# Performance work log

Hardware: AMD Instinct MI355X
Metric: run time of the kernel (lower is better)

The kernel has to match this reference:

```python
import jax, jax.numpy as jnp
import numpy as np

B, L, D, V, O = 512, 256, 256, 100000, 1000  # L must equal D (see MaxPool1d(kernel_size=D) + squeeze)


def setup_inputs() -> dict:
    key = jax.random.key(0)
    k1, k2, k3, k4, k5 = jax.random.split(key, 5)
    input_sentence = jax.random.randint(k1, (B, L), 0, V)
    emb_weight = jax.random.normal(k2, (V, D), dtype=jnp.float32) * 0.02
    # xavier_uniform for W_b: bound = sqrt(6/(D+D))
    bound = float(np.sqrt(6.0 / (D + D)))
    W_b = jax.random.uniform(k3, (D, D), dtype=jnp.float32, minval=-bound, maxval=bound)
    lw = float(np.sqrt(1.0 / D))
    lin_w = jax.random.uniform(k4, (O, D), dtype=jnp.float32, minval=-lw, maxval=lw)
    lin_b = jax.random.uniform(k5, (O,), dtype=jnp.float32, minval=-lw, maxval=lw)
    return {"input_sentence": input_sentence, "emb_weight": emb_weight,
            "W_b": W_b, "lin_w": lin_w, "lin_b": lin_b}


def reference(input_sentence, emb_weight, W_b, lin_w, lin_b):
    # Embedding lookup: [B, L, D]
    we = emb_weight[input_sentence]
    # torch stores embeddings as [B, D, L] then re-transposes inside the co-attention;
    # net effect: C = tanh(E W_b E^T) with E = [B, L, D]  ->  C: [B, L, L]
    C = jnp.tanh(jnp.einsum('bld,de,bme->blm', we, W_b, we))
    # Dropout(p=0.5) is identity in eval mode.
    # MaxPool1d(kernel_size=D) over last axis with L == D -> max over last dim, keepdims
    max_cow = jnp.max(C, axis=-1, keepdims=True)          # [B, L, 1]
    a_q = jax.nn.softmax(max_cow, axis=1)                  # softmax over L
    # bmm(a_q^T [B,1,L], E [B,L,D]) -> [B,1,D], then squeeze dim 1
    f_w = jnp.einsum('blo,bld->bod', a_q, we)[:, 0, :]     # [B, D]
    return f_w @ lin_w.T + lin_b                           # [B, O]
```

## Files before the change

### kernel.cpp

```cpp
#include <hip/hip_runtime.h>
#include <hip/hip_bf16.h>
#include <math.h>

#define B_ 512
#define L_ 256
#define D_ 256
#define V_ 100000
#define O_ 1000

typedef __attribute__((ext_vector_type(8))) short short8;
typedef __attribute__((ext_vector_type(4))) float f32x4;

static __device__ __forceinline__ unsigned short f2bf(float f) {
    union { float f; unsigned u; } v; v.f = f;
    unsigned r = v.u + 0x7FFFu + ((v.u >> 16) & 1u);
    return (unsigned short)(r >> 16);
}
static __device__ __forceinline__ float bf2f(unsigned short u) {
    union { unsigned u; float f; } v; v.u = ((unsigned)u) << 16;
    return v.f;
}

__global__ __launch_bounds__(256) void k_wt(const float* __restrict__ Wb,
                                            unsigned short* __restrict__ Wbf) {
    int i = blockIdx.x * 256 + threadIdx.x;
    Wbf[i] = f2bf(Wb[i]);
}

__global__ __launch_bounds__(512, 2) void k_attn(const int* __restrict__ tok,
                                                 const float* __restrict__ emb,
                                                 const unsigned short* __restrict__ Wbf,
                                                 float* __restrict__ fw) {
    __shared__ char lds[163840];
    char* EsC = lds;
    char* HtC = lds + 131072;
    float* red2    = (float*)(lds + 131072);
    float* scratch = (float*)(lds + 131072 + 1024);
    float* fred    = (float*)(lds + 131072 + 1152);

    int b = blockIdx.x;
    int tid = threadIdx.x;
    int wid = tid >> 6, ln = tid & 63;
    int l16 = ln & 15, gp = ln >> 4;

    {
        const int* tb = tok + (b << 8);
#pragma unroll
        for (int it = 0; it < 32; it++) {
            int row = it * 8 + wid;
            int t = tb[row];
            float4 v = *(const float4*)(emb + ((size_t)t << 8) + (ln << 2));
            unsigned long long pk;
            unsigned short* p = (unsigned short*)&pk;
            p[0] = f2bf(v.x); p[1] = f2bf(v.y); p[2] = f2bf(v.z); p[3] = f2bf(v.w);
            int byt = (row << 9) | ((ln << 3) ^ ((row & 7) << 4));
            *(unsigned long long*)(EsC + byt) = pk;
        }
    }

    int i0 = wid * 32;
    short8 wfr[8][2];
#pragma unroll
    for (int k = 0; k < 8; k++)
#pragma unroll
        for (int rf = 0; rf < 2; rf++)
            wfr[k][rf] = *(const short8*)(Wbf + ((i0 + rf * 16 + l16) << 8) + k * 32 + gp * 8);
    __syncthreads();

    int l0 = i0;
    short8 efr[8][2];
#pragma unroll
    for (int k = 0; k < 8; k++)
#pragma unroll
        for (int rf = 0; rf < 2; rf++) {
            int l = l0 + rf * 16 + l16;
            int byt = (l << 9) | ((k * 64 + gp * 16) ^ ((l & 7) << 4));
            efr[k][rf] = *(const short8*)(EsC + byt);
        }

    float rmax[8];
#pragma unroll
    for (int i = 0; i < 8; i++) rmax[i] = -1e30f;

    for (int mt = 0; mt < 4; mt++) {
        int m0 = mt * 64;
        {
            f32x4 acc[2][4] = {};
#pragma unroll
            for (int k0 = 0; k0 < 256; k0 += 32) {
                int kk2 = (k0 + gp * 8) * 2;
                short8 bfr[4];
#pragma unroll
                for (int cf = 0; cf < 4; cf++) {
                    int jg = m0 + cf * 16 + l16;
                    int byt = (jg << 9) | (kk2 ^ ((jg & 7) << 4));
                    bfr[cf] = *(const short8*)(EsC + byt);
                }
                int ks = k0 >> 5;
#pragma unroll
                for (int rf = 0; rf < 2; rf++)
#pragma unroll
                    for (int cf = 0; cf < 4; cf++)
                        acc[rf][cf] = __builtin_amdgcn_mfma_f32_16x16x32_bf16(
                            wfr[ks][rf], bfr[cf], acc[rf][cf], 0, 0, 0);
            }
#pragma unroll
            for (int rf = 0; rf < 2; rf++)
#pragma unroll
                for (int cf = 0; cf < 4; cf++) {
                    int i = i0 + rf * 16 + gp * 4;
                    int jl = cf * 16 + l16;
                    unsigned long long pk;
                    unsigned short* p = (unsigned short*)&pk;
                    p[0] = f2bf(acc[rf][cf][0]);
                    p[1] = f2bf(acc[rf][cf][1]);
                    p[2] = f2bf(acc[rf][cf][2]);
                    p[3] = f2bf(acc[rf][cf][3]);
                    int byt = (jl << 9) | ((i * 2) ^ ((jl & 7) << 4));
                    *(unsigned long long*)(HtC + byt) = pk;
                }
        }
        __syncthreads();
        {
            f32x4 acc[2][4] = {};
#pragma unroll
            for (int k0 = 0; k0 < 256; k0 += 32) {
                int kk2 = (k0 + gp * 8) * 2;
                short8 bb[4];
#pragma unroll
                for (int cf = 0; cf < 4; cf++) {
                    int m = cf * 16 + l16;
                    int byt = (m << 9) | (kk2 ^ ((m & 7) << 4));
                    bb[cf] = *(const short8*)(HtC + byt);
                }
                int ks = k0 >> 5;
#pragma unroll
                for (int rf = 0; rf < 2; rf++)
#pragma unroll
                    for (int cf = 0; cf < 4; cf++)
                        acc[rf][cf] = __builtin_amdgcn_mfma_f32_16x16x32_bf16(
                            efr[ks][rf], bb[cf], acc[rf][cf], 0, 0, 0);
            }
#pragma unroll
            for (int rf = 0; rf < 2; rf++)
#pragma unroll
                for (int r = 0; r < 4; r++) {
                    float mx = fmaxf(fmaxf(acc[rf][0][r], acc[rf][1][r]),
                                     fmaxf(acc[rf][2][r], acc[rf][3][r]));
                    rmax[rf * 4 + r] = fmaxf(rmax[rf * 4 + r], mx);
                }
        }
        __syncthreads();
    }

#pragma unroll
    for (int i = 0; i < 8; i++) {
        float v = rmax[i];
        v = fmaxf(v, __shfl_xor(v, 1));
        v = fmaxf(v, __shfl_xor(v, 2));
        v = fmaxf(v, __shfl_xor(v, 4));
        v = fmaxf(v, __shfl_xor(v, 8));
        rmax[i] = v;
    }
    if (l16 == 0) {
#pragma unroll
        for (int rf = 0; rf < 2; rf++)
#pragma unroll
            for (int r = 0; r < 4; r++)
                red2[l0 + rf * 16 + gp * 4 + r] = rmax[rf * 4 + r];
    }
    __syncthreads();

    float x = -1e30f;
    if (tid < 256) x = tanhf(red2[tid]);
    float mx = x;
#pragma unroll
    for (int s = 1; s < 64; s <<= 1) mx = fmaxf(mx, __shfl_xor(mx, s));
    if (ln == 0) scratch[wid] = mx;
    __syncthreads();
    float bm = scratch[0];
#pragma unroll
    for (int i = 1; i < 8; i++) bm = fmaxf(bm, scratch[i]);
    float e = (tid < 256) ? expf(x - bm) : 0.f;
    float sm = e;
#pragma unroll
    for (int s = 1; s < 64; s <<= 1) sm += __shfl_xor(sm, s);
    if (ln == 0) scratch[8 + wid] = sm;
    __syncthreads();
    float tot = 0.f;
#pragma unroll
    for (int i = 0; i < 8; i++) tot += scratch[8 + i];
    if (tid < 256) red2[tid] = e / tot;
    __syncthreads();

    {
        int g = tid >> 5;
        int d0 = (tid & 31) << 3;
        float s0[8] = {0.f, 0.f, 0.f, 0.f, 0.f, 0.f, 0.f, 0.f};
        int lbase = g << 4;
#pragma unroll
        for (int li = 0; li < 16; li++) {
            int l = lbase + li;
            float aql = red2[l];
            int byt = (l << 9) | ((d0 * 2) ^ ((l & 7) << 4));
            short8 v = *(const short8*)(EsC + byt);
#pragma unroll
            for (int jj = 0; jj < 8; jj++)
                s0[jj] += aql * bf2f((unsigned short)v[jj]);
        }
        f32x4 w0, w1;
        w0[0] = s0[0]; w0[1] = s0[1]; w0[2] = s0[2]; w0[3] = s0[3];
        w1[0] = s0[4]; w1[1] = s0[5]; w1[2] = s0[6]; w1[3] = s0[7];
        *(f32x4*)(fred + g * 256 + d0) = w0;
        *(f32x4*)(fred + g * 256 + d0 + 4) = w1;
    }
    __syncthreads();
    if (tid < 256) {
        float f = 0.f;
#pragma unroll
        for (int g2 = 0; g2 < 16; g2++) f += fred[g2 * 256 + tid];
        fw[(b << 8) + tid] = f;
    }
}

__global__ __launch_bounds__(256) void k_out(const float* __restrict__ fw,
                                             const float* __restrict__ lw,
                                             const float* __restrict__ lb,
                                             float* __restrict__ out) {
    __shared__ float As[32][68];
    __shared__ float Bs[64][65];
    int tid = threadIdx.x;
    int tx = tid & 15, ty = tid >> 4;
    int r0 = blockIdx.y * 32, n0 = blockIdx.x * 64;
    float acc[2][4] = {};
    for (int k0 = 0; k0 < 256; k0 += 64) {
        __syncthreads();
#pragma unroll
        for (int it = 0; it < 2; it++) {
            int idx = it * 256 + tid;
            int i = idx >> 4, k4 = (idx & 15) << 2;
            *(float4*)&As[i][k4] = *(const float4*)&fw[(r0 + i) * 256 + k0 + k4];
        }
#pragma unroll
        for (int it = 0; it < 4; it++) {
            int idx = it * 256 + tid;
            int n = idx >> 4, k4 = (idx & 15) << 2;
            int nn = n0 + n;
            float4 v = {0.f, 0.f, 0.f, 0.f};
            if (nn < O_) v = *(const float4*)&lw[(size_t)nn * 256 + k0 + k4];
            Bs[k4][n] = v.x; Bs[k4 + 1][n] = v.y; Bs[k4 + 2][n] = v.z; Bs[k4 + 3][n] = v.w;
        }
        __syncthreads();
#pragma unroll
        for (int k = 0; k < 64; k++) {
            float a0 = As[ty * 2][k], a1 = As[ty * 2 + 1][k];
            float b0 = Bs[k][tx * 4], b1 = Bs[k][tx * 4 + 1];
            float b2 = Bs[k][tx * 4 + 2], b3 = Bs[k][tx * 4 + 3];
            acc[0][0] += a0 * b0; acc[0][1] += a0 * b1; acc[0][2] += a0 * b2; acc[0][3] += a0 * b3;
            acc[1][0] += a1 * b0; acc[1][1] += a1 * b1; acc[1][2] += a1 * b2; acc[1][3] += a1 * b3;
        }
    }
#pragma unroll
    for (int i = 0; i < 2; i++)
#pragma unroll
        for (int j = 0; j < 4; j++) {
            int n = n0 + tx * 4 + j;
            if (n < O_) out[(size_t)(r0 + ty * 2 + i) * O_ + n] = acc[i][j] + lb[n];
        }
}

extern "C" void kernel_launch(void* const* d_in, const int* in_sizes, int n_in,
                              void* d_out, int out_size, void* d_ws, size_t ws_size,
                              hipStream_t stream) {
    const int* tok = (const int*)d_in[0];
    const float* emb = (const float*)d_in[1];
    const float* Wb = (const float*)d_in[2];
    const float* lw = (const float*)d_in[3];
    const float* lb = (const float*)d_in[4];
    float* out = (float*)d_out;

    char* ws = (char*)d_ws;
    unsigned short* Wbf = (unsigned short*)(ws);
    float*          fwp = (float*)(ws + 131072);

    hipLaunchKernelGGL(k_wt,   dim3(256),    dim3(256), 0, stream, Wb, Wbf);
    hipLaunchKernelGGL(k_attn, dim3(512),    dim3(512), 0, stream, tok, emb, Wbf, fwp);
    hipLaunchKernelGGL(k_out,  dim3(16, 16), dim3(256), 0, stream, fwp, lw, lb, out);
}
```

Measured before the change: 79.87 us.

## Stream embedding tiles through double-buffered LDS and prefetch next tile during compute

Instead of staging all 256 embedding rows in LDS up front, the kernel loads 64-row tiles into a double buffer, prefetching the next tile's gather into registers while the current tile's MFMAs run. One barrier per tile is removed. The A-operand fragments now come straight from global memory with bf16 conversion, and the final weighted sum re-reads fp32 embeddings from global. This cuts LDS use, from 160KB to about 145KB, and hides gather latency. In exchange it adds global re-reads and register pressure, and the final pooling now uses fp32 rather than bf16 values.

```diff
diff --git a/kernel.cpp b/kernel.cpp
--- a/kernel.cpp
+++ b/kernel.cpp
@@ -31,59 +31,76 @@
                                                  const float* __restrict__ emb,
                                                  const unsigned short* __restrict__ Wbf,
                                                  float* __restrict__ fw) {
-    __shared__ char lds[163840];
-    char* EsC = lds;
-    char* HtC = lds + 131072;
+    __shared__ __align__(16) char lds[148544];
     float* red2    = (float*)(lds + 131072);
-    float* scratch = (float*)(lds + 131072 + 1024);
-    float* fred    = (float*)(lds + 131072 + 1152);
+    float* scratch = (float*)(lds + 132096);
+    float* fred    = (float*)(lds + 132160);
 
     int b = blockIdx.x;
     int tid = threadIdx.x;
     int wid = tid >> 6, ln = tid & 63;
     int l16 = ln & 15, gp = ln >> 4;
-
-    {
-        const int* tb = tok + (b << 8);
-#pragma unroll
-        for (int it = 0; it < 32; it++) {
-            int row = it * 8 + wid;
-            int t = tb[row];
-            float4 v = *(const float4*)(emb + ((size_t)t << 8) + (ln << 2));
-            unsigned long long pk;
-            unsigned short* p = (unsigned short*)&pk;
-            p[0] = f2bf(v.x); p[1] = f2bf(v.y); p[2] = f2bf(v.z); p[3] = f2bf(v.w);
-            int byt = (row << 9) | ((ln << 3) ^ ((row & 7) << 4));
-            *(unsigned long long*)(EsC + byt) = pk;
-        }
-    }
-
     int i0 = wid * 32;
+    const int* tb = tok + (b << 8);
+
+    float4 g4[8];
+#pragma unroll
+    for (int it = 0; it < 8; it++) {
+        int r = it * 8 + wid;
+        g4[it] = *(const float4*)(emb + ((size_t)tb[r] << 8) + (ln << 2));
+    }
     short8 wfr[8][2];
 #pragma unroll
     for (int k = 0; k < 8; k++)
 #pragma unroll
         for (int rf = 0; rf < 2; rf++)
             wfr[k][rf] = *(const short8*)(Wbf + ((i0 + rf * 16 + l16) << 8) + k * 32 + gp * 8);
-    __syncthreads();
-
-    int l0 = i0;
+    int trow0 = tb[i0 + l16];
+    int trow1 = tb[i0 + 16 + l16];
     short8 efr[8][2];
 #pragma unroll
     for (int k = 0; k < 8; k++)
 #pragma unroll
         for (int rf = 0; rf < 2; rf++) {
-            int l = l0 + rf * 16 + l16;
-            int byt = (l << 9) | ((k * 64 + gp * 16) ^ ((l & 7) << 4));
-            efr[k][rf] = *(const short8*)(EsC + byt);
-        }
+            const float4* sp = (const float4*)(emb + ((size_t)(rf ? trow1 : trow0) << 8) + k * 32 + gp * 8);
+            float4 a = sp[0], c = sp[1];
+            short8 o;
+            o[0] = (short)f2bf(a.x); o[1] = (short)f2bf(a.y);
+            o[2] = (short)f2bf(a.z); o[3] = (short)f2bf(a.w);
+            o[4] = (short)f2bf(c.x); o[5] = (short)f2bf(c.y);
+            o[6] = (short)f2bf(c.z); o[7] = (short)f2bf(c.w);
+            efr[k][rf] = o;
+        }
+#pragma unroll
+    for (int it = 0; it < 8; it++) {
+        int r = it * 8 + wid;
+        unsigned long long pk;
+        unsigned short* p = (unsigned short*)&pk;
+        p[0] = f2bf(g4[it].x); p[1] = f2bf(g4[it].y);
+        p[2] = f2bf(g4[it].z); p[3] = f2bf(g4[it].w);
+        *(unsigned long long*)(lds + ((r << 9) | ((ln << 3) ^ ((r & 7) << 4)))) = pk;
+    }
+    __syncthreads();
 
     float rmax[8];
 #pragma unroll
     for (int i = 0; i < 8; i++) rmax[i] = -1e30f;
 
+#pragma unroll
     for (int mt = 0; mt < 4; mt++) {
-        int m0 = mt * 64;
+        char* EtCur = lds + (mt & 1) * 32768;
+        char* EtNxt = lds + ((mt + 1) & 1) * 32768;
+        char* HtCur = lds + 65536 + (mt & 1) * 32768;
+
+        float4 ng[8];
+        if (mt < 3) {
+            int m0n = (mt + 1) * 64;
+#pragma unroll
+            for (int it = 0; it < 8; it++) {
+                int r = it * 8 + wid;
+                ng[it] = *(const float4*)(emb + ((size_t)tb[m0n + r] << 8) + (ln << 2));
+            }
+        }
         {
             f32x4 acc[2][4] = {};
 #pragma unroll
@@ -92,9 +109,8 @@
                 short8 bfr[4];
 #pragma unroll
                 for (int cf = 0; cf < 4; cf++) {
-                    int jg = m0 + cf * 16 + l16;
-                    int byt = (jg << 9) | (kk2 ^ ((jg & 7) << 4));
-                    bfr[cf] = *(const short8*)(EsC + byt);
+                    int jl = cf * 16 + l16;
+                    bfr[cf] = *(const short8*)(EtCur + ((jl << 9) | (kk2 ^ ((jl & 7) << 4))));
                 }
                 int ks = k0 >> 5;
 #pragma unroll
@@ -116,9 +132,19 @@
                     p[1] = f2bf(acc[rf][cf][1]);
                     p[2] = f2bf(acc[rf][cf][2]);
                     p[3] = f2bf(acc[rf][cf][3]);
-                    int byt = (jl << 9) | ((i * 2) ^ ((jl & 7) << 4));
-                    *(unsigned long long*)(HtC + byt) = pk;
+                    *(unsigned long long*)(HtCur + ((jl << 9) | ((i * 2) ^ ((jl & 7) << 4)))) = pk;
                 }
+        }
+        if (mt < 3) {
+#pragma unroll
+            for (int it = 0; it < 8; it++) {
+                int r = it * 8 + wid;
+                unsigned long long pk;
+                unsigned short* p = (unsigned short*)&pk;
+                p[0] = f2bf(ng[it].x); p[1] = f2bf(ng[it].y);
+                p[2] = f2bf(ng[it].z); p[3] = f2bf(ng[it].w);
+                *(unsigned long long*)(EtNxt + ((r << 9) | ((ln << 3) ^ ((r & 7) << 4)))) = pk;
+            }
         }
         __syncthreads();
         {
@@ -130,8 +156,7 @@
 #pragma unroll
                 for (int cf = 0; cf < 4; cf++) {
                     int m = cf * 16 + l16;
-                    int byt = (m << 9) | (kk2 ^ ((m & 7) << 4));
-                    bb[cf] = *(const short8*)(HtC + byt);
+                    bb[cf] = *(const short8*)(HtCur + ((m << 9) | (kk2 ^ ((m & 7) << 4))));
                 }
                 int ks = k0 >> 5;
 #pragma unroll
@@ -150,7 +175,6 @@
                     rmax[rf * 4 + r] = fmaxf(rmax[rf * 4 + r], mx);
                 }
         }
-        __syncthreads();
     }
 
 #pragma unroll
@@ -167,7 +191,7 @@
         for (int rf = 0; rf < 2; rf++)
 #pragma unroll
             for (int r = 0; r < 4; r++)
-                red2[l0 + rf * 16 + gp * 4 + r] = rmax[rf * 4 + r];
+                red2[i0 + rf * 16 + gp * 4 + r] = rmax[rf * 4 + r];
     }
     __syncthreads();
 
@@ -202,11 +226,10 @@
         for (int li = 0; li < 16; li++) {
             int l = lbase + li;
             float aql = red2[l];
-            int byt = (l << 9) | ((d0 * 2) ^ ((l & 7) << 4));
-            short8 v = *(const short8*)(EsC + byt);
-#pragma unroll
-            for (int jj = 0; jj < 8; jj++)
-                s0[jj] += aql * bf2f((unsigned short)v[jj]);
+            const float4* sp = (const float4*)(emb + ((size_t)tb[l] << 8) + d0);
+            float4 a = sp[0], c = sp[1];
+            s0[0] += aql * a.x; s0[1] += aql * a.y; s0[2] += aql * a.z; s0[3] += aql * a.w;
+            s0[4] += aql * c.x; s0[5] += aql * c.y; s0[6] += aql * c.z; s0[7] += aql * c.w;
         }
         f32x4 w0, w1;
         w0[0] = s0[0]; w0[1] = s0[1]; w0[2] = s0[2]; w0[3] = s0[3];
```

After: 131.2 us. 1.64x slower.

## Overlap embedding gather with first GEMM tile and swizzle reduction buffer

Applied to the files above, without the earlier changes.

The embedding gather is split up. The first 64 rows are loaded and packed before the first W_b·E^T tile, which depends only on them. The remaining rows are fetched in flight, with part held in registers across that first tile's MFMA work, then packed into LDS afterward. This hides global-memory latency behind compute. It also adds s_setprio around the MFMA blocks, 16-byte vector gather stores, and an XOR swizzle on the fred reduction buffer to cut LDS bank conflicts. The cost is higher register pressure from the 12 prefetched float4s, which could hurt occupancy or cause spills.

```diff
diff --git a/kernel.cpp b/kernel.cpp
--- a/kernel.cpp
+++ b/kernel.cpp
@@ -20,6 +20,15 @@
     union { unsigned u; float f; } v; v.u = ((unsigned)u) << 16;
     return v.f;
 }
+static __device__ __forceinline__ short8 pack8(float4 a, float4 c) {
+    short8 o;
+    o[0] = (short)f2bf(a.x); o[1] = (short)f2bf(a.y);
+    o[2] = (short)f2bf(a.z); o[3] = (short)f2bf(a.w);
+    o[4] = (short)f2bf(c.x); o[5] = (short)f2bf(c.y);
+    o[6] = (short)f2bf(c.z); o[7] = (short)f2bf(c.w);
+    return o;
+}
+static __device__ __forceinline__ int fsw(int d) { return d ^ (((d >> 5) & 7) << 2); }
 
 __global__ __launch_bounds__(256) void k_wt(const float* __restrict__ Wb,
                                             unsigned short* __restrict__ Wbf) {
@@ -31,125 +40,153 @@
                                                  const float* __restrict__ emb,
                                                  const unsigned short* __restrict__ Wbf,
                                                  float* __restrict__ fw) {
-    __shared__ char lds[163840];
+    __shared__ __align__(16) char lds[163840];
     char* EsC = lds;
     char* HtC = lds + 131072;
     float* red2    = (float*)(lds + 131072);
-    float* scratch = (float*)(lds + 131072 + 1024);
-    float* fred    = (float*)(lds + 131072 + 1152);
+    float* scratch = (float*)(lds + 132096);
+    float* fred    = (float*)(lds + 132160);
 
     int b = blockIdx.x;
     int tid = threadIdx.x;
     int wid = tid >> 6, ln = tid & 63;
     int l16 = ln & 15, gp = ln >> 4;
-
-    {
-        const int* tb = tok + (b << 8);
-#pragma unroll
-        for (int it = 0; it < 32; it++) {
-            int row = it * 8 + wid;
-            int t = tb[row];
-            float4 v = *(const float4*)(emb + ((size_t)t << 8) + (ln << 2));
-            unsigned long long pk;
-            unsigned short* p = (unsigned short*)&pk;
-            p[0] = f2bf(v.x); p[1] = f2bf(v.y); p[2] = f2bf(v.z); p[3] = f2bf(v.w);
-            int byt = (row << 9) | ((ln << 3) ^ ((row & 7) << 4));
-            *(unsigned long long*)(EsC + byt) = pk;
-        }
-    }
-
     int i0 = wid * 32;
+    const int* tb = tok + (b << 8);
+
     short8 wfr[8][2];
 #pragma unroll
     for (int k = 0; k < 8; k++)
 #pragma unroll
         for (int rf = 0; rf < 2; rf++)
             wfr[k][rf] = *(const short8*)(Wbf + ((i0 + rf * 16 + l16) << 8) + k * 32 + gp * 8);
-    __syncthreads();
-
-    int l0 = i0;
+
+#pragma unroll
+    for (int it = 0; it < 4; it++) {
+        int c = it * 512 + tid;
+        int row = c >> 5, c16 = c & 31;
+        const float4* src = (const float4*)(emb + ((size_t)tb[row] << 8) + (c16 << 3));
+        short8 o = pack8(src[0], src[1]);
+        *(short8*)(EsC + ((row << 9) | ((c16 << 4) ^ ((row & 7) << 4)))) = o;
+    }
+    __syncthreads();
+
+    float4 ga[6], gb[6];
+#pragma unroll
+    for (int it = 0; it < 6; it++) {
+        int c = (it + 4) * 512 + tid;
+        int row = c >> 5, c16 = c & 31;
+        const float4* src = (const float4*)(emb + ((size_t)tb[row] << 8) + (c16 << 3));
+        ga[it] = src[0]; gb[it] = src[1];
+    }
+
+    float rmax[8];
+#pragma unroll
+    for (int i = 0; i < 8; i++) rmax[i] = -1e30f;
+
+    auto P1 = [&](int m0) {
+        f32x4 acc[2][4] = {};
+#pragma unroll
+        for (int k0 = 0; k0 < 256; k0 += 32) {
+            int kk2 = (k0 + gp * 8) * 2;
+            short8 bfr[4];
+#pragma unroll
+            for (int cf = 0; cf < 4; cf++) {
+                int jg = m0 + cf * 16 + l16;
+                bfr[cf] = *(const short8*)(EsC + ((jg << 9) | (kk2 ^ ((jg & 7) << 4))));
+            }
+            int ks = k0 >> 5;
+            __builtin_amdgcn_s_setprio(1);
+#pragma unroll
+            for (int rf = 0; rf < 2; rf++)
+#pragma unroll
+                for (int cf = 0; cf < 4; cf++)
+                    acc[rf][cf] = __builtin_amdgcn_mfma_f32_16x16x32_bf16(
+                        wfr[ks][rf], bfr[cf], acc[rf][cf], 0, 0, 0);
+            __builtin_amdgcn_s_setprio(0);
+        }
+#pragma unroll
+        for (int rf = 0; rf < 2; rf++)
+#pragma unroll
+            for (int cf = 0; cf < 4; cf++) {
+                int i = i0 + rf * 16 + gp * 4;
+                int jl = cf * 16 + l16;
+                unsigned long long pk;
+                unsigned short* p = (unsigned short*)&pk;
+                p[0] = f2bf(acc[rf][cf][0]);
+                p[1] = f2bf(acc[rf][cf][1]);
+                p[2] = f2bf(acc[rf][cf][2]);
+                p[3] = f2bf(acc[rf][cf][3]);
+                *(unsigned long long*)(HtC + ((jl << 9) | ((i * 2) ^ ((jl & 7) << 4)))) = pk;
+            }
+    };
+
     short8 efr[8][2];
+    auto P2 = [&]() {
+        f32x4 acc[2][4] = {};
+#pragma unroll
+        for (int k0 = 0; k0 < 256; k0 += 32) {
+            int kk2 = (k0 + gp * 8) * 2;
+            short8 bb[4];
+#pragma unroll
+            for (int cf = 0; cf < 4; cf++) {
+                int m = cf * 16 + l16;
+                bb[cf] = *(const short8*)(HtC + ((m << 9) | (kk2 ^ ((m & 7) << 4))));
+            }
+            int ks = k0 >> 5;
+            __builtin_amdgcn_s_setprio(1);
+#pragma unroll
+            for (int rf = 0; rf < 2; rf++)
+#pragma unroll
+                for (int cf = 0; cf < 4; cf++)
+                    acc[rf][cf] = __builtin_amdgcn_mfma_f32_16x16x32_bf16(
+                        efr[ks][rf], bb[cf], acc[rf][cf], 0, 0, 0);
+            __builtin_amdgcn_s_setprio(0);
+        }
+#pragma unroll
+        for (int rf = 0; rf < 2; rf++)
+#pragma unroll
+            for (int r = 0; r < 4; r++) {
+                float mx = fmaxf(fmaxf(acc[rf][0][r], acc[rf][1][r]),
+                                 fmaxf(acc[rf][2][r], acc[rf][3][r]));
+                rmax[rf * 4 + r] = fmaxf(rmax[rf * 4 + r], mx);
+            }
+    };
+
+    P1(0);
+
+#pragma unroll
+    for (int it = 0; it < 6; it++) {
+        int c = (it + 4) * 512 + tid;
+        int row = c >> 5, c16 = c & 31;
+        short8 o = pack8(ga[it], gb[it]);
+        *(short8*)(EsC + ((row << 9) | ((c16 << 4) ^ ((row & 7) << 4)))) = o;
+    }
+#pragma unroll
+    for (int it = 10; it < 16; it++) {
+        int c = it * 512 + tid;
+        int row = c >> 5, c16 = c & 31;
+        const float4* src = (const float4*)(emb + ((size_t)tb[row] << 8) + (c16 << 3));
+        short8 o = pack8(src[0], src[1]);
+        *(short8*)(EsC + ((row << 9) | ((c16 << 4) ^ ((row & 7) << 4)))) = o;
+    }
+    __syncthreads();
+
 #pragma unroll
     for (int k = 0; k < 8; k++)
 #pragma unroll
         for (int rf = 0; rf < 2; rf++) {
-            int l = l0 + rf * 16 + l16;
-            int byt = (l << 9) | ((k * 64 + gp * 16) ^ ((l & 7) << 4));
-            efr[k][rf] = *(const short8*)(EsC + byt);
-        }
-
-    float rmax[8];
-#pragma unroll
-    for (int i = 0; i < 8; i++) rmax[i] = -1e30f;
-
-    for (int mt = 0; mt < 4; mt++) {
-        int m0 = mt * 64;
-        {
-            f32x4 acc[2][4] = {};
-#pragma unroll
-            for (int k0 = 0; k0 < 256; k0 += 32) {
-                int kk2 = (k0 + gp * 8) * 2;
-                short8 bfr[4];
-#pragma unroll
-                for (int cf = 0; cf < 4; cf++) {
-                    int jg = m0 + cf * 16 + l16;
-                    int byt = (jg << 9) | (kk2 ^ ((jg & 7) << 4));
-                    bfr[cf] = *(const short8*)(EsC + byt);
-                }
-                int ks = k0 >> 5;
-#pragma unroll
-                for (int rf = 0; rf < 2; rf++)
-#pragma unroll
-                    for (int cf = 0; cf < 4; cf++)
-                        acc[rf][cf] = __builtin_amdgcn_mfma_f32_16x16x32_bf16(
-                            wfr[ks][rf], bfr[cf], acc[rf][cf], 0, 0, 0);
-            }
-#pragma unroll
-            for (int rf = 0; rf < 2; rf++)
-#pragma unroll
-                for (int cf = 0; cf < 4; cf++) {
-                    int i = i0 + rf * 16 + gp * 4;
-                    int jl = cf * 16 + l16;
-                    unsigned long long pk;
-                    unsigned short* p = (unsigned short*)&pk;
-                    p[0] = f2bf(acc[rf][cf][0]);
-                    p[1] = f2bf(acc[rf][cf][1]);
-                    p[2] = f2bf(acc[rf][cf][2]);
-                    p[3] = f2bf(acc[rf][cf][3]);
-                    int byt = (jl << 9) | ((i * 2) ^ ((jl & 7) << 4));
-                    *(unsigned long long*)(HtC + byt) = pk;
-                }
-        }
+            int l = i0 + rf * 16 + l16;
+            efr[k][rf] = *(const short8*)(EsC + ((l << 9) | ((k * 64 + gp * 16) ^ ((l & 7) << 4))));
+        }
+
+    P2();
+    __syncthreads();
+
+    for (int mt = 1; mt < 4; mt++) {
+        P1(mt * 64);
         __syncthreads();
-        {
-            f32x4 acc[2][4] = {};
-#pragma unroll
-            for (int k0 = 0; k0 < 256; k0 += 32) {
-                int kk2 = (k0 + gp * 8) * 2;
-                short8 bb[4];
-#pragma unroll
-                for (int cf = 0; cf < 4; cf++) {
-                    int m = cf * 16 + l16;
-                    int byt = (m << 9) | (kk2 ^ ((m & 7) << 4));
-                    bb[cf] = *(const short8*)(HtC + byt);
-                }
-                int ks = k0 >> 5;
-#pragma unroll
-                for (int rf = 0; rf < 2; rf++)
-#pragma unroll
-                    for (int cf = 0; cf < 4; cf++)
-                        acc[rf][cf] = __builtin_amdgcn_mfma_f32_16x16x32_bf16(
-                            efr[ks][rf], bb[cf], acc[rf][cf], 0, 0, 0);
-            }
-#pragma unroll
-            for (int rf = 0; rf < 2; rf++)
-#pragma unroll
-                for (int r = 0; r < 4; r++) {
-                    float mx = fmaxf(fmaxf(acc[rf][0][r], acc[rf][1][r]),
-                                     fmaxf(acc[rf][2][r], acc[rf][3][r]));
-                    rmax[rf * 4 + r] = fmaxf(rmax[rf * 4 + r], mx);
-                }
-        }
+        P2();
         __syncthreads();
     }
 
@@ -167,7 +204,7 @@
         for (int rf = 0; rf < 2; rf++)
 #pragma unroll
             for (int r = 0; r < 4; r++)
-                red2[l0 + rf * 16 + gp * 4 + r] = rmax[rf * 4 + r];
+                red2[i0 + rf * 16 + gp * 4 + r] = rmax[rf * 4 + r];
     }
     __syncthreads();
 
@@ -211,14 +248,15 @@
         f32x4 w0, w1;
         w0[0] = s0[0]; w0[1] = s0[1]; w0[2] = s0[2]; w0[3] = s0[3];
         w1[0] = s0[4]; w1[1] = s0[5]; w1[2] = s0[6]; w1[3] = s0[7];
-        *(f32x4*)(fred + g * 256 + d0) = w0;
-        *(f32x4*)(fred + g * 256 + d0 + 4) = w1;
+        *(f32x4*)(fred + g * 256 + fsw(d0)) = w0;
+        *(f32x4*)(fred + g * 256 + fsw(d0 + 4)) = w1;
     }
     __syncthreads();
     if (tid < 256) {
         float f = 0.f;
-#pragma unroll
-        for (int g2 = 0; g2 < 16; g2++) f += fred[g2 * 256 + tid];
+        int dw = fsw(tid);
+#pragma unroll
+        for (int g2 = 0; g2 < 16; g2++) f += fred[g2 * 256 + dw];
         fw[(b << 8) + tid] = f;
     }
 }
```

Measured after the change: 76.38 us. 1.05x faster.
